# Performance work log

Measured on AMD Instinct MI355X. Metric: run time of the kernel, lower is better.

Reference implementation:

```python
import jax, jax.numpy as jnp
import numpy as np

NEG_SLOPE = 0.01  # torch nn.LeakyReLU default


def setup_inputs() -> dict:
    key = jax.random.key(0)
    k1, k2, k3, k4 = jax.random.split(key, 4)
    B, N, d = 256, 64, 64
    embeddings = jax.random.normal(k1, (B, N, d), dtype=jnp.float32)
    # nn.Linear(em_dim, em_dim): weight [d, d] (out, in), bias [d]
    w_W = jax.random.normal(k2, (d, d), dtype=jnp.float32) / np.sqrt(d)
    w_b = jax.random.normal(k3, (d,), dtype=jnp.float32) * 0.01
    # nn.Linear(em_dim, 1): weight [1, d] -> stored as [d], bias [1]
    a_W = jax.random.normal(k4, (d,), dtype=jnp.float32) / np.sqrt(d)
    a_b = jnp.zeros((1,), dtype=jnp.float32)
    return {"embeddings": embeddings, "w_W": w_W, "w_b": w_b, "a_W": a_W, "a_b": a_b}


def reference(embeddings, w_W, w_b, a_W, a_b):
    # pairwise elementwise product: value[b,i,j,d] = emb[b,i,d] * emb[b,j,d]
    value = embeddings[:, :, None, :] * embeddings[:, None, :, :]  # [B,N,N,d]
    # small linear d->d (torch Linear: x @ W.T + b)
    qk = jnp.einsum('bijd,ed->bije', value, w_W) + w_b
    qk = jnp.where(qk >= 0, qk, NEG_SLOPE * qk)  # LeakyReLU
    # dropout is identity in eval mode
    logits = jnp.einsum('bijd,d->bij', qk, a_W) + a_b[0]  # linear d->1, squeeze
    alphas = jax.nn.softmax(logits, axis=-1)[..., None]  # [B,N,N,1]
    return alphas, value
```

## Files before the change

kernel.cpp:

```cpp
#include <hip/hip_runtime.h>

typedef __attribute__((ext_vector_type(8))) short short8;
typedef __attribute__((ext_vector_type(4))) float floatx4;
typedef __attribute__((ext_vector_type(4))) int   intx4;

#define NEG_SLOPE 0.01f

__device__ __forceinline__ short f2bf(float f) {
    unsigned u = __float_as_uint(f);
    unsigned r = (u + 0x7FFFu + ((u >> 16) & 1u)) >> 16;
    return (short)r;
}

__device__ __forceinline__ int pack2(float x, float y) {
    return (int)(unsigned short)f2bf(x) | ((int)(unsigned short)f2bf(y) << 16);
}

__global__ __launch_bounds__(256, 2)
void afm_kernel(const float* __restrict__ emb,
                const float* __restrict__ wW,
                const float* __restrict__ wb,
                const float* __restrict__ aW,
                float* __restrict__ aOut,
                float* __restrict__ vOut) {
    __shared__ __align__(16) float sEf[64][68];
    __shared__ __align__(16) float sW [64][68];
    __shared__ __align__(16) short sEb[64][72];
    __shared__ __align__(16) float sei[4][64];
    __shared__ __align__(16) float swb[64];
    __shared__ __align__(16) float saw[64];
    __shared__ __align__(16) float slog[4][64];

    const int tid   = threadIdx.x;
    const int lane  = tid & 63;
    const int w     = tid >> 6;
    const int blk   = blockIdx.x;
    const int b     = blk >> 4;
    const int iBase = (blk & 15) << 2;
    const int i     = iBase + w;

    const float* embB = emb + (size_t)b * 4096;

    {
        int row = tid >> 2;
        int c0  = (tid & 3) << 4;
        const float* src = embB + row * 64 + c0;
        float4 a0 = *(const float4*)(src);
        float4 a1 = *(const float4*)(src + 4);
        float4 a2 = *(const float4*)(src + 8);
        float4 a3 = *(const float4*)(src + 12);
        *(float4*)&sEf[row][c0]      = a0;
        *(float4*)&sEf[row][c0 + 4]  = a1;
        *(float4*)&sEf[row][c0 + 8]  = a2;
        *(float4*)&sEf[row][c0 + 12] = a3;
        intx4 q0, q1;
        q0[0] = pack2(a0.x, a0.y); q0[1] = pack2(a0.z, a0.w);
        q0[2] = pack2(a1.x, a1.y); q0[3] = pack2(a1.z, a1.w);
        q1[0] = pack2(a2.x, a2.y); q1[1] = pack2(a2.z, a2.w);
        q1[2] = pack2(a3.x, a3.y); q1[3] = pack2(a3.z, a3.w);
        *(intx4*)&sEb[row][c0]     = q0;
        *(intx4*)&sEb[row][c0 + 8] = q1;

        const float* wsrc = wW + row * 64 + c0;
        float4 b0 = *(const float4*)(wsrc);
        float4 b1 = *(const float4*)(wsrc + 4);
        float4 b2 = *(const float4*)(wsrc + 8);
        float4 b3 = *(const float4*)(wsrc + 12);
        *(float4*)&sW[row][c0]      = b0;
        *(float4*)&sW[row][c0 + 4]  = b1;
        *(float4*)&sW[row][c0 + 8]  = b2;
        *(float4*)&sW[row][c0 + 12] = b3;

        sei[w][lane] = embB[i * 64 + lane];
        if (tid < 64)        swb[tid]       = wb[tid];
        else if (tid < 128)  saw[tid - 64]  = aW[tid - 64];
    }
    __syncthreads();

    {
        float* base = vOut + ((size_t)(b * 64 + i) << 12);
        const int joff = lane >> 4;
        const int d0   = (lane & 15) << 2;
        float4 ei = *(float4*)&sei[w][d0];
        #pragma unroll
        for (int c = 0; c < 16; ++c) {
            int j = (c << 2) + joff;
            float4 ej = *(float4*)&sEf[j][d0];
            float4 v;
            v.x = ei.x * ej.x; v.y = ei.y * ej.y;
            v.z = ei.z * ej.z; v.w = ei.w * ej.w;
            *(float4*)(base + (c << 8) + (lane << 2)) = v;
        }
    }

    const int lo = lane & 15, hi = lane >> 4;
    floatx4 acc[4][4];
    #pragma unroll
    for (int jt = 0; jt < 4; ++jt)
        #pragma unroll
        for (int et = 0; et < 4; ++et)
            acc[jt][et] = (floatx4){0.f, 0.f, 0.f, 0.f};

    #pragma unroll
    for (int kt = 0; kt < 2; ++kt) {
        const int d0 = kt * 32 + hi * 8;
        float4 ei0 = *(float4*)&sei[w][d0];
        float4 ei1 = *(float4*)&sei[w][d0 + 4];
        short8 bf[4];
        #pragma unroll
        for (int et = 0; et < 4; ++et) {
            int e = et * 16 + lo;
            float4 w0 = *(float4*)&sW[e][d0];
            float4 w1 = *(float4*)&sW[e][d0 + 4];
            short8 t;
            t[0] = f2bf(w0.x * ei0.x); t[1] = f2bf(w0.y * ei0.y);
            t[2] = f2bf(w0.z * ei0.z); t[3] = f2bf(w0.w * ei0.w);
            t[4] = f2bf(w1.x * ei1.x); t[5] = f2bf(w1.y * ei1.y);
            t[6] = f2bf(w1.z * ei1.z); t[7] = f2bf(w1.w * ei1.w);
            bf[et] = t;
        }
        #pragma unroll
        for (int jt = 0; jt < 4; ++jt) {
            short8 af = *(short8*)&sEb[jt * 16 + lo][d0];
            #pragma unroll
            for (int et = 0; et < 4; ++et)
                acc[jt][et] = __builtin_amdgcn_mfma_f32_16x16x32_bf16(
                    af, bf[et], acc[jt][et], 0, 0, 0);
        }
    }

    float wbv[4], awv[4];
    #pragma unroll
    for (int et = 0; et < 4; ++et) {
        int e = et * 16 + lo;
        wbv[et] = swb[e];
        awv[et] = saw[e];
    }

    float lg[16];
    #pragma unroll
    for (int jt = 0; jt < 4; ++jt) {
        #pragma unroll
        for (int r = 0; r < 4; ++r) {
            float p = 0.f;
            #pragma unroll
            for (int et = 0; et < 4; ++et) {
                float x = acc[jt][et][r] + wbv[et];
                x = (x >= 0.f) ? x : NEG_SLOPE * x;
                p += awv[et] * x;
            }
            p += __shfl_xor(p, 1);
            p += __shfl_xor(p, 2);
            p += __shfl_xor(p, 4);
            p += __shfl_xor(p, 8);
            lg[jt * 4 + r] = p;
        }
    }

    float m = lg[0];
    #pragma unroll
    for (int k = 1; k < 16; ++k) m = fmaxf(m, lg[k]);
    m = fmaxf(m, __shfl_xor(m, 16));
    m = fmaxf(m, __shfl_xor(m, 32));

    float ex[16];
    float s = 0.f;
    #pragma unroll
    for (int k = 0; k < 16; ++k) { ex[k] = __expf(lg[k] - m); s += ex[k]; }
    s += __shfl_xor(s, 16);
    s += __shfl_xor(s, 32);
    float inv = 1.f / s;

    if (lo == 0) {
        #pragma unroll
        for (int jt = 0; jt < 4; ++jt)
            #pragma unroll
            for (int r = 0; r < 4; ++r)
                slog[w][jt * 16 + hi * 4 + r] = ex[jt * 4 + r] * inv;
    }
    __syncthreads();
    aOut[((size_t)(b * 64 + i) << 6) + lane] = slog[w][lane];
}

extern "C" void kernel_launch(void* const* d_in, const int* in_sizes, int n_in,
                              void* d_out, int out_size, void* d_ws, size_t ws_size,
                              hipStream_t stream) {
    const float* emb = (const float*)d_in[0];
    const float* wW  = (const float*)d_in[1];
    const float* wb  = (const float*)d_in[2];
    const float* aW  = (const float*)d_in[3];
    float* aOut = (float*)d_out;
    float* vOut = aOut + (size_t)256 * 64 * 64;
    afm_kernel<<<4096, 256, 0, stream>>>(emb, wW, wb, aW, aOut, vOut);
}
```

Measured before the change: 284.3 us.

## Use 512-thread blocks, nontemporal value stores, and per-row-tile MFMA accumulation

Each block now handles 8 rows i instead of 4, halving the number of blocks and spreading the redundant per-block load of embeddings and weights over more work. The large value output is written with nontemporal stores to avoid polluting caches. The MFMA accumulators are restructured to run one j-tile at a time, which cuts live accumulator registers so a higher occupancy target fits, and LeakyReLU becomes a fmax. The cost is larger blocks with more shared memory per block, which may limit scheduling flexibility.

```diff
diff --git a/kernel.cpp b/kernel.cpp
--- a/kernel.cpp
+++ b/kernel.cpp
@@ -16,7 +16,7 @@
     return (int)(unsigned short)f2bf(x) | ((int)(unsigned short)f2bf(y) << 16);
 }
 
-__global__ __launch_bounds__(256, 2)
+__global__ __launch_bounds__(512, 4)
 void afm_kernel(const float* __restrict__ emb,
                 const float* __restrict__ wW,
                 const float* __restrict__ wb,
@@ -26,50 +26,39 @@
     __shared__ __align__(16) float sEf[64][68];
     __shared__ __align__(16) float sW [64][68];
     __shared__ __align__(16) short sEb[64][72];
-    __shared__ __align__(16) float sei[4][64];
+    __shared__ __align__(16) float sei[8][64];
     __shared__ __align__(16) float swb[64];
     __shared__ __align__(16) float saw[64];
-    __shared__ __align__(16) float slog[4][64];
+    __shared__ __align__(16) float slog[8][64];
 
     const int tid   = threadIdx.x;
     const int lane  = tid & 63;
     const int w     = tid >> 6;
     const int blk   = blockIdx.x;
-    const int b     = blk >> 4;
-    const int iBase = (blk & 15) << 2;
+    const int b     = blk >> 3;
+    const int iBase = (blk & 7) << 3;
     const int i     = iBase + w;
 
     const float* embB = emb + (size_t)b * 4096;
 
     {
-        int row = tid >> 2;
-        int c0  = (tid & 3) << 4;
+        int row = tid >> 3;
+        int c0  = (tid & 7) << 3;
         const float* src = embB + row * 64 + c0;
         float4 a0 = *(const float4*)(src);
         float4 a1 = *(const float4*)(src + 4);
-        float4 a2 = *(const float4*)(src + 8);
-        float4 a3 = *(const float4*)(src + 12);
-        *(float4*)&sEf[row][c0]      = a0;
-        *(float4*)&sEf[row][c0 + 4]  = a1;
-        *(float4*)&sEf[row][c0 + 8]  = a2;
-        *(float4*)&sEf[row][c0 + 12] = a3;
-        intx4 q0, q1;
-        q0[0] = pack2(a0.x, a0.y); q0[1] = pack2(a0.z, a0.w);
-        q0[2] = pack2(a1.x, a1.y); q0[3] = pack2(a1.z, a1.w);
-        q1[0] = pack2(a2.x, a2.y); q1[1] = pack2(a2.z, a2.w);
-        q1[2] = pack2(a3.x, a3.y); q1[3] = pack2(a3.z, a3.w);
-        *(intx4*)&sEb[row][c0]     = q0;
-        *(intx4*)&sEb[row][c0 + 8] = q1;
+        *(float4*)&sEf[row][c0]     = a0;
+        *(float4*)&sEf[row][c0 + 4] = a1;
+        intx4 q;
+        q[0] = pack2(a0.x, a0.y); q[1] = pack2(a0.z, a0.w);
+        q[2] = pack2(a1.x, a1.y); q[3] = pack2(a1.z, a1.w);
+        *(intx4*)&sEb[row][c0] = q;
 
         const float* wsrc = wW + row * 64 + c0;
         float4 b0 = *(const float4*)(wsrc);
         float4 b1 = *(const float4*)(wsrc + 4);
-        float4 b2 = *(const float4*)(wsrc + 8);
-        float4 b3 = *(const float4*)(wsrc + 12);
-        *(float4*)&sW[row][c0]      = b0;
-        *(float4*)&sW[row][c0 + 4]  = b1;
-        *(float4*)&sW[row][c0 + 8]  = b2;
-        *(float4*)&sW[row][c0 + 12] = b3;
+        *(float4*)&sW[row][c0]     = b0;
+        *(float4*)&sW[row][c0 + 4] = b1;
 
         sei[w][lane] = embB[i * 64 + lane];
         if (tid < 64)        swb[tid]       = wb[tid];
@@ -86,27 +75,21 @@
         for (int c = 0; c < 16; ++c) {
             int j = (c << 2) + joff;
             float4 ej = *(float4*)&sEf[j][d0];
-            float4 v;
-            v.x = ei.x * ej.x; v.y = ei.y * ej.y;
-            v.z = ei.z * ej.z; v.w = ei.w * ej.w;
-            *(float4*)(base + (c << 8) + (lane << 2)) = v;
+            floatx4 v;
+            v[0] = ei.x * ej.x; v[1] = ei.y * ej.y;
+            v[2] = ei.z * ej.z; v[3] = ei.w * ej.w;
+            __builtin_nontemporal_store(v, (floatx4*)(base + (c << 8) + (lane << 2)));
         }
     }
 
     const int lo = lane & 15, hi = lane >> 4;
-    floatx4 acc[4][4];
-    #pragma unroll
-    for (int jt = 0; jt < 4; ++jt)
-        #pragma unroll
-        for (int et = 0; et < 4; ++et)
-            acc[jt][et] = (floatx4){0.f, 0.f, 0.f, 0.f};
 
+    short8 bf[2][4];
     #pragma unroll
     for (int kt = 0; kt < 2; ++kt) {
         const int d0 = kt * 32 + hi * 8;
         float4 ei0 = *(float4*)&sei[w][d0];
         float4 ei1 = *(float4*)&sei[w][d0 + 4];
-        short8 bf[4];
         #pragma unroll
         for (int et = 0; et < 4; ++et) {
             int e = et * 16 + lo;
@@ -117,15 +100,7 @@
             t[2] = f2bf(w0.z * ei0.z); t[3] = f2bf(w0.w * ei0.w);
             t[4] = f2bf(w1.x * ei1.x); t[5] = f2bf(w1.y * ei1.y);
             t[6] = f2bf(w1.z * ei1.z); t[7] = f2bf(w1.w * ei1.w);
-            bf[et] = t;
-        }
-        #pragma unroll
-        for (int jt = 0; jt < 4; ++jt) {
-            short8 af = *(short8*)&sEb[jt * 16 + lo][d0];
-            #pragma unroll
-            for (int et = 0; et < 4; ++et)
-                acc[jt][et] = __builtin_amdgcn_mfma_f32_16x16x32_bf16(
-                    af, bf[et], acc[jt][et], 0, 0, 0);
+            bf[kt][et] = t;
         }
     }
 
@@ -140,13 +115,25 @@
     float lg[16];
     #pragma unroll
     for (int jt = 0; jt < 4; ++jt) {
+        floatx4 acc[4];
+        #pragma unroll
+        for (int et = 0; et < 4; ++et)
+            acc[et] = (floatx4){0.f, 0.f, 0.f, 0.f};
+        #pragma unroll
+        for (int kt = 0; kt < 2; ++kt) {
+            short8 af = *(short8*)&sEb[jt * 16 + lo][kt * 32 + hi * 8];
+            #pragma unroll
+            for (int et = 0; et < 4; ++et)
+                acc[et] = __builtin_amdgcn_mfma_f32_16x16x32_bf16(
+                    af, bf[kt][et], acc[et], 0, 0, 0);
+        }
         #pragma unroll
         for (int r = 0; r < 4; ++r) {
             float p = 0.f;
             #pragma unroll
             for (int et = 0; et < 4; ++et) {
-                float x = acc[jt][et][r] + wbv[et];
-                x = (x >= 0.f) ? x : NEG_SLOPE * x;
+                float x = acc[et][r] + wbv[et];
+                x = fmaxf(x, NEG_SLOPE * x);
                 p += awv[et] * x;
             }
             p += __shfl_xor(p, 1);
@@ -191,5 +178,5 @@
     const float* aW  = (const float*)d_in[3];
     float* aOut = (float*)d_out;
     float* vOut = aOut + (size_t)256 * 64 * 64;
-    afm_kernel<<<4096, 256, 0, stream>>>(emb, wW, wb, aW, aOut, vOut);
+    afm_kernel<<<2048, 512, 0, stream>>>(emb, wW, wb, aW, aOut, vOut);
 }
```

Result: no change. 279.5 us (-1.7%).

## Split value-tensor store and attention compute into separate specialized blocks

Applied to the files above, without the earlier changes.

Doubles the grid so that even blocks only write the pairwise product tensor, using nontemporal stores, while odd blocks only do the MFMA attention-logit and softmax path. The write-heavy and compute-heavy work now run in different blocks, and shared memory is unioned into one buffer. The MFMA loop is restructured so only one row-tile's accumulators are live at a time, occupancy is raised to 4 blocks per SM, and LeakyReLU becomes a fmax. In exchange, the embedding tile is loaded twice and a divergent branch decides each block's role.

```diff
diff --git a/kernel.cpp b/kernel.cpp
--- a/kernel.cpp
+++ b/kernel.cpp
@@ -16,30 +16,63 @@
     return (int)(unsigned short)f2bf(x) | ((int)(unsigned short)f2bf(y) << 16);
 }
 
-__global__ __launch_bounds__(256, 2)
+__global__ __launch_bounds__(256, 4)
 void afm_kernel(const float* __restrict__ emb,
                 const float* __restrict__ wW,
                 const float* __restrict__ wb,
                 const float* __restrict__ aW,
                 float* __restrict__ aOut,
                 float* __restrict__ vOut) {
-    __shared__ __align__(16) float sEf[64][68];
-    __shared__ __align__(16) float sW [64][68];
-    __shared__ __align__(16) short sEb[64][72];
-    __shared__ __align__(16) float sei[4][64];
-    __shared__ __align__(16) float swb[64];
-    __shared__ __align__(16) float saw[64];
-    __shared__ __align__(16) float slog[4][64];
-
-    const int tid   = threadIdx.x;
-    const int lane  = tid & 63;
-    const int w     = tid >> 6;
-    const int blk   = blockIdx.x;
-    const int b     = blk >> 4;
-    const int iBase = (blk & 15) << 2;
-    const int i     = iBase + w;
+    __shared__ __align__(16) char smem[29184];
+
+    const int tid = threadIdx.x;
+    const int blk = blockIdx.x;
+    const int g   = blk >> 1;
+    const int b   = g >> 4;
+    const int iq  = g & 15;
 
     const float* embB = emb + (size_t)b * 4096;
+
+    if ((blk & 1) == 0) {
+        float (*sE)[64] = (float (*)[64])smem;
+        #pragma unroll
+        for (int k = 0; k < 4; ++k) {
+            int f4 = k * 256 + tid;
+            float4 x = *(const float4*)(embB + (f4 << 2));
+            *(float4*)&sE[0][f4 << 2] = x;
+        }
+        __syncthreads();
+
+        const int d0 = (tid & 15) << 2;
+        const int jb = tid >> 4;
+        floatx4 ei[4];
+        #pragma unroll
+        for (int il = 0; il < 4; ++il)
+            ei[il] = *(floatx4*)&sE[iq * 4 + il][d0];
+
+        #pragma unroll
+        for (int c = 0; c < 16; ++c) {
+            const int il = c >> 2;
+            const int j  = ((c & 3) << 4) + jb;
+            floatx4 ej = *(floatx4*)&sE[j][d0];
+            floatx4 x  = ei[il] * ej;
+            float* dst = vOut + ((size_t)(b * 64 + iq * 4 + il) << 12)
+                              + ((c & 3) << 10) + (tid << 2);
+            __builtin_nontemporal_store(x, (floatx4*)dst);
+        }
+        return;
+    }
+
+    float (*sW)[68]   = (float (*)[68])smem;
+    short (*sEb)[72]  = (short (*)[72])(smem + 17408);
+    float (*sei)[64]  = (float (*)[64])(smem + 26624);
+    float *swb        = (float *)(smem + 27648);
+    float *saw        = (float *)(smem + 27904);
+    float (*slog)[64] = (float (*)[64])(smem + 28160);
+
+    const int lane = tid & 63;
+    const int w    = tid >> 6;
+    const int i    = iq * 4 + w;
 
     {
         int row = tid >> 2;
@@ -49,10 +82,6 @@
         float4 a1 = *(const float4*)(src + 4);
         float4 a2 = *(const float4*)(src + 8);
         float4 a3 = *(const float4*)(src + 12);
-        *(float4*)&sEf[row][c0]      = a0;
-        *(float4*)&sEf[row][c0 + 4]  = a1;
-        *(float4*)&sEf[row][c0 + 8]  = a2;
-        *(float4*)&sEf[row][c0 + 12] = a3;
         intx4 q0, q1;
         q0[0] = pack2(a0.x, a0.y); q0[1] = pack2(a0.z, a0.w);
         q0[2] = pack2(a1.x, a1.y); q0[3] = pack2(a1.z, a1.w);
@@ -77,36 +106,14 @@
     }
     __syncthreads();
 
-    {
-        float* base = vOut + ((size_t)(b * 64 + i) << 12);
-        const int joff = lane >> 4;
-        const int d0   = (lane & 15) << 2;
-        float4 ei = *(float4*)&sei[w][d0];
-        #pragma unroll
-        for (int c = 0; c < 16; ++c) {
-            int j = (c << 2) + joff;
-            float4 ej = *(float4*)&sEf[j][d0];
-            float4 v;
-            v.x = ei.x * ej.x; v.y = ei.y * ej.y;
-            v.z = ei.z * ej.z; v.w = ei.w * ej.w;
-            *(float4*)(base + (c << 8) + (lane << 2)) = v;
-        }
-    }
-
     const int lo = lane & 15, hi = lane >> 4;
-    floatx4 acc[4][4];
-    #pragma unroll
-    for (int jt = 0; jt < 4; ++jt)
-        #pragma unroll
-        for (int et = 0; et < 4; ++et)
-            acc[jt][et] = (floatx4){0.f, 0.f, 0.f, 0.f};
-
+
+    short8 bf[2][4];
     #pragma unroll
     for (int kt = 0; kt < 2; ++kt) {
         const int d0 = kt * 32 + hi * 8;
         float4 ei0 = *(float4*)&sei[w][d0];
         float4 ei1 = *(float4*)&sei[w][d0 + 4];
-        short8 bf[4];
         #pragma unroll
         for (int et = 0; et < 4; ++et) {
             int e = et * 16 + lo;
@@ -117,15 +124,7 @@
             t[2] = f2bf(w0.z * ei0.z); t[3] = f2bf(w0.w * ei0.w);
             t[4] = f2bf(w1.x * ei1.x); t[5] = f2bf(w1.y * ei1.y);
             t[6] = f2bf(w1.z * ei1.z); t[7] = f2bf(w1.w * ei1.w);
-            bf[et] = t;
-        }
-        #pragma unroll
-        for (int jt = 0; jt < 4; ++jt) {
-            short8 af = *(short8*)&sEb[jt * 16 + lo][d0];
-            #pragma unroll
-            for (int et = 0; et < 4; ++et)
-                acc[jt][et] = __builtin_amdgcn_mfma_f32_16x16x32_bf16(
-                    af, bf[et], acc[jt][et], 0, 0, 0);
+            bf[kt][et] = t;
         }
     }
 
@@ -140,13 +139,25 @@
     float lg[16];
     #pragma unroll
     for (int jt = 0; jt < 4; ++jt) {
+        floatx4 acc[4];
+        #pragma unroll
+        for (int et = 0; et < 4; ++et)
+            acc[et] = (floatx4){0.f, 0.f, 0.f, 0.f};
+        #pragma unroll
+        for (int kt = 0; kt < 2; ++kt) {
+            short8 af = *(short8*)&sEb[jt * 16 + lo][kt * 32 + hi * 8];
+            #pragma unroll
+            for (int et = 0; et < 4; ++et)
+                acc[et] = __builtin_amdgcn_mfma_f32_16x16x32_bf16(
+                    af, bf[kt][et], acc[et], 0, 0, 0);
+        }
         #pragma unroll
         for (int r = 0; r < 4; ++r) {
             float p = 0.f;
             #pragma unroll
             for (int et = 0; et < 4; ++et) {
-                float x = acc[jt][et][r] + wbv[et];
-                x = (x >= 0.f) ? x : NEG_SLOPE * x;
+                float x = acc[et][r] + wbv[et];
+                x = fmaxf(x, NEG_SLOPE * x);
                 p += awv[et] * x;
             }
             p += __shfl_xor(p, 1);
@@ -191,5 +202,5 @@
     const float* aW  = (const float*)d_in[3];
     float* aOut = (float*)d_out;
     float* vOut = aOut + (size_t)256 * 64 * 64;
-    afm_kernel<<<4096, 256, 0, stream>>>(emb, wW, wb, aW, aOut, vOut);
-}
+    afm_kernel<<<8192, 256, 0, stream>>>(emb, wW, wb, aW, aOut, vOut);
+}
```

After: 289.4 us. No clear change (+1.8%).
